# Kernel optimization log

Measured on AMD Instinct MI355X. Metric: run time of the kernel, lower is better.

Reference implementation:

```python
import jax, jax.numpy as jnp
import numpy as np

N = 50000
E = 800000
EPS = 1e-5

def _gcn_conv(x, src, dst, norm, W, b):
    # PyG GCNConv: linear transform, normalized gather/scatter, then bias.
    xw = x @ W                                   # [N, out]
    msgs = xw[src] * norm[:, None]               # [E+N, out] gather
    out = jax.ops.segment_sum(msgs, dst, num_segments=N)  # scatter-add
    return out + b

def _bn_eval(x, gamma, beta, mean, var):
    return (x - mean) * jax.lax.rsqrt(var + EPS) * gamma + beta

def setup_inputs() -> dict:
    key = jax.random.key(0)
    ks = jax.random.split(key, 24)
    dims = [(128, 256), (256, 128), (128, 64), (64, 6)]
    inp = {
        "x": jax.random.normal(ks[0], (N, 128), dtype=jnp.float32),
        "edge_index": jax.random.randint(ks[1], (2, E), 0, N, dtype=jnp.int64),
    }
    i = 2
    for li, (fi, fo) in enumerate(dims, start=1):
        scale = 1.0 / np.sqrt(fi)
        inp[f"W{li}"] = jax.random.uniform(ks[i], (fi, fo), jnp.float32, -scale, scale); i += 1
        inp[f"b{li}"] = jnp.zeros((fo,), jnp.float32)
        if li < 4:  # BN after first three convs
            inp[f"g{li}"] = jnp.ones((fo,), jnp.float32)
            inp[f"be{li}"] = jnp.zeros((fo,), jnp.float32)
            inp[f"m{li}"] = 0.1 * jax.random.normal(ks[i], (fo,), jnp.float32); i += 1
            inp[f"v{li}"] = jax.random.uniform(ks[i], (fo,), jnp.float32, 0.5, 1.5); i += 1
    return inp

def reference(x, edge_index,
              W1, b1, g1, be1, m1, v1,
              W2, b2, g2, be2, m2, v2,
              W3, b3, g3, be3, m3, v3,
              W4, b4):
    # Add self-loops once; symmetric normalization deg^-1/2 (with self-loops).
    loops = jnp.arange(N, dtype=edge_index.dtype)
    src = jnp.concatenate([edge_index[0], loops])
    dst = jnp.concatenate([edge_index[1], loops])
    deg = jax.ops.segment_sum(jnp.ones_like(dst, dtype=x.dtype), dst, num_segments=N)
    dinv = jnp.where(deg > 0, jax.lax.rsqrt(deg), 0.0)
    norm = dinv[src] * dinv[dst]  # [E+N]

    h = _gcn_conv(x, src, dst, norm, W1, b1)
    h = jax.nn.relu(_bn_eval(h, g1, be1, m1, v1))  # dropout: no-op in eval
    h = _gcn_conv(h, src, dst, norm, W2, b2)
    h = jax.nn.relu(_bn_eval(h, g2, be2, m2, v2))
    h = _gcn_conv(h, src, dst, norm, W3, b3)
    h = jax.nn.relu(_bn_eval(h, g3, be3, m3, v3))
    return _gcn_conv(h, src, dst, norm, W4, b4)
```

## Files before the change

kernel.cpp:

```cpp
#include <hip/hip_runtime.h>
#include <hip/hip_bf16.h>
#include <hip/hip_fp16.h>

#define EPS 1e-5f

constexpr int NN = 50000;
constexpr int NE = 800000;

typedef __attribute__((ext_vector_type(8))) __bf16 bf16x8;
typedef __attribute__((ext_vector_type(4))) float f32x4;

__global__ void memset_i32(int* p, int n) {
  int i = blockIdx.x * blockDim.x + threadIdx.x;
  if (i < n) p[i] = 0;
}

__global__ void deg_pos(const int* __restrict__ dst, int* __restrict__ degi,
                        unsigned char* __restrict__ pos8, int n) {
  int i = blockIdx.x * blockDim.x + threadIdx.x;
  if (i < n) pos8[i] = (unsigned char)atomicAdd(&degi[dst[i]], 1);
}

__global__ __launch_bounds__(1024) void scan1(const int* __restrict__ cnt,
                                              int* __restrict__ incl,
                                              int* __restrict__ bsum, int n) {
  __shared__ int s[1024];
  int tid = threadIdx.x;
  int i = blockIdx.x * 1024 + tid;
  int v = (i < n) ? cnt[i] : 0;
  s[tid] = v;
  __syncthreads();
  for (int off = 1; off < 1024; off <<= 1) {
    int t = (tid >= off) ? s[tid - off] : 0;
    __syncthreads();
    s[tid] += t;
    __syncthreads();
  }
  if (i < n) incl[i] = s[tid];
  if (tid == 1023) bsum[blockIdx.x] = s[1023];
}

__global__ void scan2(int* __restrict__ bsum, int nb) {
  int lane = threadIdx.x;
  int v = (lane < nb) ? bsum[lane] : 0;
  int orig = v;
  for (int off = 1; off < 64; off <<= 1) {
    int t = __shfl_up(v, off, 64);
    if (lane >= off) v += t;
  }
  if (lane < nb) bsum[lane] = v - orig;
}

__global__ __launch_bounds__(1024) void scan3(const int* __restrict__ cnt,
                                              const int* __restrict__ incl,
                                              const int* __restrict__ bsum,
                                              int* __restrict__ rp,
                                              float* __restrict__ dinv, int n) {
  int tid = threadIdx.x;
  int i = blockIdx.x * 1024 + tid;
  if (i < n) {
    rp[i + 1] = incl[i] + bsum[blockIdx.x];
    dinv[i] = rsqrtf((float)(cnt[i] + 1));
  }
  if (i == 0) rp[0] = 0;
}

__global__ void fill_kernel(const int* __restrict__ src, const int* __restrict__ dst,
                            const int* __restrict__ rp,
                            const unsigned char* __restrict__ pos8,
                            unsigned short* __restrict__ col, int n) {
  int i = blockIdx.x * blockDim.x + threadIdx.x;
  if (i < n) col[rp[dst[i]] + pos8[i]] = (unsigned short)src[i];
}

__device__ __forceinline__ void wsplit_one(const float* W, __bf16* th, __bf16* tl,
                                           int j, int K, int N) {
  int k = j / N, n = j - k * N;
  float v = W[j];
  __bf16 h = (__bf16)v;
  th[(size_t)n * K + k] = h;
  tl[(size_t)n * K + k] = (__bf16)(v - (float)h);
}

__global__ void wsplit_scale(const float* __restrict__ W1, __bf16* t1h, __bf16* t1l,
                             const float* __restrict__ W2, __bf16* t2h, __bf16* t2l,
                             const float* __restrict__ W3, __bf16* t3h, __bf16* t3l,
                             const float* __restrict__ W4, __bf16* t4h, __bf16* t4l,
                             const float* __restrict__ x, const float* __restrict__ dinv,
                             __half* __restrict__ Xh) {
  int i = blockIdx.x * blockDim.x + threadIdx.x;
  if (i < 32768) { wsplit_one(W1, t1h, t1l, i, 128, 256); return; }
  if (i < 65536) { wsplit_one(W2, t2h, t2l, i - 32768, 256, 128); return; }
  if (i < 73728) { wsplit_one(W3, t3h, t3l, i - 65536, 128, 64); return; }
  if (i < 74112) { wsplit_one(W4, t4h, t4l, i - 73728, 64, 6); return; }
  int k = i - 74112;
  if (k >= NN * 32) return;
  int v = k >> 5, f = (k & 31) * 4;
  float4 t = ((const float4*)x)[k];
  float s = dinv[v];
  __half2* d = (__half2*)(Xh + (size_t)v * 128 + f);
  d[0] = __floats2half2_rn(t.x * s, t.y * s);
  d[1] = __floats2half2_rn(t.z * s, t.w * s);
}

template <int F, int EPI>
__global__ __launch_bounds__(256, 8) void prop_half(
    const __half* __restrict__ in, const int* __restrict__ rp,
    const unsigned short* __restrict__ col,
    const float* __restrict__ dinv, const float* __restrict__ bias,
    const float* __restrict__ gam, const float* __restrict__ bet,
    const float* __restrict__ mean, const float* __restrict__ var,
    __bf16* __restrict__ out_hi, __bf16* __restrict__ out_lo, int nnodes) {
  int tid = threadIdx.x;
  int wid = tid >> 6, lane = tid & 63;
  constexpr int VEC = F / 64;
  int v = blockIdx.x * 4 + wid;
  if (v >= nnodes) return;
  int e0 = rp[v], e1 = rp[v + 1];
  float acc[VEC];
  if constexpr (VEC == 2) {
    float2 f = __half22float2(*(const __half2*)(in + (size_t)v * F + lane * 2));
    acc[0] = f.x; acc[1] = f.y;
  } else {
    acc[0] = __half2float(in[(size_t)v * F + lane]);
  }
  int e1m1 = e1 - 1;
  constexpr int D = 8;
  for (int e = e0; e < e1; e += D) {
    bool full = (e + D <= e1);
    int ss[D];
    if (full) {
#pragma unroll
      for (int u = 0; u < D; u++) ss[u] = col[e + u];
      if constexpr (VEC == 2) {
        __half2 hv[D];
#pragma unroll
        for (int u = 0; u < D; u++)
          hv[u] = *(const __half2*)(in + (size_t)ss[u] * F + lane * 2);
#pragma unroll
        for (int u = 0; u < D; u++) {
          float2 f = __half22float2(hv[u]);
          acc[0] += f.x;
          acc[1] += f.y;
        }
      } else {
        __half hv[D];
#pragma unroll
        for (int u = 0; u < D; u++) hv[u] = in[(size_t)ss[u] * F + lane];
#pragma unroll
        for (int u = 0; u < D; u++) acc[0] += __half2float(hv[u]);
      }
    } else {
      float w[D];
#pragma unroll
      for (int u = 0; u < D; u++) {
        int ei = e + u;
        ss[u] = col[ei < e1m1 ? ei : e1m1];
        w[u] = (ei < e1) ? 1.f : 0.f;
      }
      if constexpr (VEC == 2) {
        __half2 hv[D];
#pragma unroll
        for (int u = 0; u < D; u++)
          hv[u] = *(const __half2*)(in + (size_t)ss[u] * F + lane * 2);
#pragma unroll
        for (int u = 0; u < D; u++) {
          float2 f = __half22float2(hv[u]);
          acc[0] = fmaf(f.x, w[u], acc[0]);
          acc[1] = fmaf(f.y, w[u], acc[1]);
        }
      } else {
        __half hv[D];
#pragma unroll
        for (int u = 0; u < D; u++) hv[u] = in[(size_t)ss[u] * F + lane];
#pragma unroll
        for (int u = 0; u < D; u++) acc[0] = fmaf(__half2float(hv[u]), w[u], acc[0]);
      }
    }
  }
  float dv = dinv[v];
#pragma unroll
  for (int j = 0; j < VEC; j++) {
    int f = lane * VEC + j;
    float t = acc[j] * dv;
    if constexpr (EPI >= 1) {
      t += bias[f];
      t = (t - mean[f]) * rsqrtf(var[f] + EPS) * gam[f] + bet[f];
      t = fmaxf(t, 0.f);
    }
    __bf16 h = (__bf16)t;
    out_hi[(size_t)v * F + f] = h;
    out_lo[(size_t)v * F + f] = (__bf16)(t - (float)h);
  }
}

__global__ __launch_bounds__(256, 8) void prop_small(
    const float* __restrict__ in, const int* __restrict__ rp,
    const unsigned short* __restrict__ col,
    const float* __restrict__ dinv, const float* __restrict__ bias,
    float* __restrict__ out, int nnodes) {
  constexpr int F = 6;
  int tid = threadIdx.x;
  int wid = tid >> 6, lane = tid & 63;
  int g = lane >> 3, f = lane & 7;
  int v = (blockIdx.x * 4 + wid) * 8 + g;
  if (v >= nnodes || f >= F) return;
  int e0 = rp[v], e1 = rp[v + 1];
  float acc = in[(size_t)v * F + f];
  int e1m1 = e1 - 1;
  constexpr int D = 8;
  for (int e = e0; e < e1; e += D) {
    int ss[D];
    float w[D];
#pragma unroll
    for (int u = 0; u < D; u++) {
      int ei = e + u;
      ss[u] = col[ei < e1m1 ? ei : e1m1];
      w[u] = (ei < e1) ? 1.0f : 0.0f;
    }
#pragma unroll
    for (int u = 0; u < D; u++) acc = fmaf(in[(size_t)ss[u] * F + f], w[u], acc);
  }
  out[(size_t)v * F + f] = acc * dinv[v] + bias[f];
}

template <int BN, int EPI>
__global__ __launch_bounds__(256, 4) void mfma_gemm(
    const __bf16* __restrict__ Ahi, const __bf16* __restrict__ Alo,
    const __bf16* __restrict__ Bhi, const __bf16* __restrict__ Blo,
    const float* __restrict__ bias, const float* __restrict__ gam,
    const float* __restrict__ bet, const float* __restrict__ mean,
    const float* __restrict__ var, const float* __restrict__ dinv,
    float* __restrict__ Cf, __half* __restrict__ Ch,
    __bf16* __restrict__ Chi, __bf16* __restrict__ Clo,
    int M, int K, int N) {
  constexpr int BM = 128, BK = 32, NB = BN / 16;
  __shared__ __bf16 Ah[BM][BK + 8], Al[BM][BK + 8];
  __shared__ __bf16 Bh[BN][BK + 8], Bl[BN][BK + 8];
  int tid = threadIdx.x;
  int wid = tid >> 6, lane = tid & 63;
  int lr = lane & 15, lg = lane >> 4;
  int bm = blockIdx.x * BM, bn = blockIdx.y * BN;
  f32x4 acc[2][NB] = {};
  for (int k0 = 0; k0 < K; k0 += BK) {
#pragma unroll
    for (int c = 0; c < 2; c++) {
      int idx = tid + c * 256;
      int r = idx >> 2, s = idx & 3;
      int rg = bm + r;
      uint4 vh = {0, 0, 0, 0}, vl = {0, 0, 0, 0};
      if (rg < M) {
        size_t go = (size_t)rg * K + k0 + s * 8;
        vh = *reinterpret_cast<const uint4*>(Ahi + go);
        vl = *reinterpret_cast<const uint4*>(Alo + go);
      }
      *reinterpret_cast<uint4*>(&Ah[r][s * 8]) = vh;
      *reinterpret_cast<uint4*>(&Al[r][s * 8]) = vl;
    }
#pragma unroll
    for (int c = 0; c < (BN * 4 + 255) / 256; c++) {
      int idx = tid + c * 256;
      if (idx < BN * 4) {
        int r = idx >> 2, s = idx & 3;
        int rg = bn + r;
        uint4 vh = {0, 0, 0, 0}, vl = {0, 0, 0, 0};
        if (rg < N) {
          size_t go = (size_t)rg * K + k0 + s * 8;
          vh = *reinterpret_cast<const uint4*>(Bhi + go);
          vl = *reinterpret_cast<const uint4*>(Blo + go);
        }
        *reinterpret_cast<uint4*>(&Bh[r][s * 8]) = vh;
        *reinterpret_cast<uint4*>(&Bl[r][s * 8]) = vl;
      }
    }
    __syncthreads();
    int ar = wid * 32 + lr;
    bf16x8 ah0 = *reinterpret_cast<const bf16x8*>(&Ah[ar][lg * 8]);
    bf16x8 ah1 = *reinterpret_cast<const bf16x8*>(&Ah[ar + 16][lg * 8]);
    bf16x8 al0 = *reinterpret_cast<const bf16x8*>(&Al[ar][lg * 8]);
    bf16x8 al1 = *reinterpret_cast<const bf16x8*>(&Al[ar + 16][lg * 8]);
#pragma unroll
    for (int n = 0; n < NB; n++) {
      bf16x8 bh = *reinterpret_cast<const bf16x8*>(&Bh[n * 16 + lr][lg * 8]);
      bf16x8 bl = *reinterpret_cast<const bf16x8*>(&Bl[n * 16 + lr][lg * 8]);
      acc[0][n] = __builtin_amdgcn_mfma_f32_16x16x32_bf16(ah0, bh, acc[0][n], 0, 0, 0);
      acc[1][n] = __builtin_amdgcn_mfma_f32_16x16x32_bf16(ah1, bh, acc[1][n], 0, 0, 0);
      acc[0][n] = __builtin_amdgcn_mfma_f32_16x16x32_bf16(ah0, bl, acc[0][n], 0, 0, 0);
      acc[1][n] = __builtin_amdgcn_mfma_f32_16x16x32_bf16(ah1, bl, acc[1][n], 0, 0, 0);
      acc[0][n] = __builtin_amdgcn_mfma_f32_16x16x32_bf16(al0, bh, acc[0][n], 0, 0, 0);
      acc[1][n] = __builtin_amdgcn_mfma_f32_16x16x32_bf16(al1, bh, acc[1][n], 0, 0, 0);
    }
    __syncthreads();
  }
#pragma unroll
  for (int m = 0; m < 2; m++) {
    int row0 = bm + wid * 32 + m * 16 + lg * 4;
#pragma unroll
    for (int n = 0; n < NB; n++) {
      int colg = bn + n * 16 + lr;
#pragma unroll
      for (int r = 0; r < 4; r++) {
        int row = row0 + r;
        if (row >= M) continue;
        float t = acc[m][n][r];
        if constexpr (EPI == 0) {
          t += bias[colg];
          t = (t - mean[colg]) * rsqrtf(var[colg] + EPS) * gam[colg] + bet[colg];
          t = fmaxf(t, 0.f);
          __bf16 h = (__bf16)t;
          Chi[(size_t)row * N + colg] = h;
          Clo[(size_t)row * N + colg] = (__bf16)(t - (float)h);
        } else if constexpr (EPI == 1) {
          Ch[(size_t)row * N + colg] = __float2half(t * dinv[row]);
        } else {
          if (colg < N) Cf[(size_t)row * N + colg] = t * dinv[row];
        }
      }
    }
  }
}

extern "C" void kernel_launch(void* const* d_in, const int* in_sizes, int n_in,
                              void* d_out, int out_size, void* d_ws, size_t ws_size,
                              hipStream_t stream) {
  const float* x = (const float*)d_in[0];
  const int* ei = (const int*)d_in[1];
  const int* esrc = ei;
  const int* edst = ei + NE;
  const float* W1 = (const float*)d_in[2];  const float* b1 = (const float*)d_in[3];
  const float* g1 = (const float*)d_in[4];  const float* be1 = (const float*)d_in[5];
  const float* m1 = (const float*)d_in[6];  const float* v1 = (const float*)d_in[7];
  const float* W2 = (const float*)d_in[8];  const float* b2 = (const float*)d_in[9];
  const float* g2 = (const float*)d_in[10]; const float* be2 = (const float*)d_in[11];
  const float* m2 = (const float*)d_in[12]; const float* v2 = (const float*)d_in[13];
  const float* W3 = (const float*)d_in[14]; const float* b3 = (const float*)d_in[15];
  const float* g3 = (const float*)d_in[16]; const float* be3 = (const float*)d_in[17];
  const float* m3 = (const float*)d_in[18]; const float* v3 = (const float*)d_in[19];
  const float* W4 = (const float*)d_in[20]; const float* b4 = (const float*)d_in[21];
  float* out = (float*)d_out;

  char* base = (char*)d_ws;
  size_t off = 0;
  auto alloc = [&](size_t bytes) {
    void* p = base + off;
    off = (off + bytes + 255) & ~(size_t)255;
    return p;
  };
  __half* Xh = (__half*)alloc((size_t)NN * 128 * 2);
  float* F1 = (float*)alloc((size_t)NN * 6 * 4);
  __bf16* PAh = (__bf16*)alloc((size_t)NN * 128 * 2);
  __bf16* PAl = (__bf16*)alloc((size_t)NN * 128 * 2);
  __bf16* PHh = (__bf16*)alloc((size_t)NN * 256 * 2);
  __bf16* PHl = (__bf16*)alloc((size_t)NN * 256 * 2);
  __bf16* Wt1h = (__bf16*)alloc(128 * 256 * 2); __bf16* Wt1l = (__bf16*)alloc(128 * 256 * 2);
  __bf16* Wt2h = (__bf16*)alloc(256 * 128 * 2); __bf16* Wt2l = (__bf16*)alloc(256 * 128 * 2);
  __bf16* Wt3h = (__bf16*)alloc(128 * 64 * 2);  __bf16* Wt3l = (__bf16*)alloc(128 * 64 * 2);
  __bf16* Wt4h = (__bf16*)alloc(64 * 6 * 2);    __bf16* Wt4l = (__bf16*)alloc(64 * 6 * 2);
  int* degi = (int*)alloc((size_t)NN * 4);
  float* dinv = (float*)alloc((size_t)NN * 4);
  int* rp = (int*)alloc((size_t)(NN + 1) * 4);
  int* incl = (int*)alloc((size_t)NN * 4);
  int* bsum = (int*)alloc(64 * 4);
  unsigned short* col = (unsigned short*)alloc((size_t)NE * 2);
  unsigned char* pos8 = (unsigned char*)alloc((size_t)NE);

  const int nBlkN = (NN + 255) / 256;
  const int nBlkE = (NE + 255) / 256;
  const int nBlkScan = (NN + 1023) / 1024;
  const int gM = (NN + 127) / 128;
  const int gP = (NN + 3) / 4;

  memset_i32<<<nBlkN, 256, 0, stream>>>(degi, NN);
  deg_pos<<<nBlkE, 256, 0, stream>>>(edst, degi, pos8, NE);
  scan1<<<nBlkScan, 1024, 0, stream>>>(degi, incl, bsum, NN);
  scan2<<<1, 64, 0, stream>>>(bsum, nBlkScan);
  scan3<<<nBlkScan, 1024, 0, stream>>>(degi, incl, bsum, rp, dinv, NN);
  fill_kernel<<<nBlkE, 256, 0, stream>>>(esrc, edst, rp, pos8, col, NE);

  wsplit_scale<<<(74112 + NN * 32 + 255) / 256, 256, 0, stream>>>(
      W1, Wt1h, Wt1l, W2, Wt2h, Wt2l, W3, Wt3h, Wt3l, W4, Wt4h, Wt4l, x, dinv, Xh);

  prop_half<128, 0><<<gP, 256, 0, stream>>>(Xh, rp, col, dinv, nullptr, nullptr, nullptr,
                                            nullptr, nullptr, PAh, PAl, NN);
  {
    dim3 g(gM, 2);
    mfma_gemm<128, 0><<<g, 256, 0, stream>>>(PAh, PAl, Wt1h, Wt1l, b1, g1, be1, m1, v1,
                                             nullptr, nullptr, nullptr, PHh, PHl,
                                             NN, 128, 256);
  }
  {
    dim3 g(gM, 1);
    mfma_gemm<128, 1><<<g, 256, 0, stream>>>(PHh, PHl, Wt2h, Wt2l, nullptr, nullptr,
                                             nullptr, nullptr, nullptr, dinv,
                                             nullptr, Xh, nullptr, nullptr, NN, 256, 128);
  }
  prop_half<128, 1><<<gP, 256, 0, stream>>>(Xh, rp, col, dinv, b2, g2, be2, m2, v2,
                                            PAh, PAl, NN);
  {
    dim3 g(gM, 1);
    mfma_gemm<64, 1><<<g, 256, 0, stream>>>(PAh, PAl, Wt3h, Wt3l, nullptr, nullptr,
                                            nullptr, nullptr, nullptr, dinv,
                                            nullptr, Xh, nullptr, nullptr, NN, 128, 64);
  }
  prop_half<64, 1><<<gP, 256, 0, stream>>>(Xh, rp, col, dinv, b3, g3, be3, m3, v3,
                                           PHh, PHl, NN);
  {
    dim3 g(gM, 1);
    mfma_gemm<16, 2><<<g, 256, 0, stream>>>(PHh, PHl, Wt4h, Wt4l, nullptr, nullptr,
                                            nullptr, nullptr, nullptr, dinv,
                                            F1, nullptr, nullptr, nullptr, NN, 64, 6);
  }
  prop_small<<<(NN + 31) / 32, 256, 0, stream>>>(F1, rp, col, dinv, b4, out, NN);
}
```

Before: 256.6 us.

## Switch activations to single fp16 and use fp16 MFMA with split weights

After: 237.6 us. 1.08x faster.

```diff
diff --git a/kernel.cpp b/kernel.cpp
--- a/kernel.cpp
+++ b/kernel.cpp
@@ -7,7 +7,7 @@
 constexpr int NN = 50000;
 constexpr int NE = 800000;
 
-typedef __attribute__((ext_vector_type(8))) __bf16 bf16x8;
+typedef __attribute__((ext_vector_type(8))) _Float16 f16x8;
 typedef __attribute__((ext_vector_type(4))) float f32x4;
 
 __global__ void memset_i32(int* p, int n) {
@@ -73,19 +73,19 @@
   if (i < n) col[rp[dst[i]] + pos8[i]] = (unsigned short)src[i];
 }
 
-__device__ __forceinline__ void wsplit_one(const float* W, __bf16* th, __bf16* tl,
+__device__ __forceinline__ void wsplit_one(const float* W, __half* th, __half* tl,
                                            int j, int K, int N) {
   int k = j / N, n = j - k * N;
   float v = W[j];
-  __bf16 h = (__bf16)v;
+  __half h = __float2half(v);
   th[(size_t)n * K + k] = h;
-  tl[(size_t)n * K + k] = (__bf16)(v - (float)h);
-}
-
-__global__ void wsplit_scale(const float* __restrict__ W1, __bf16* t1h, __bf16* t1l,
-                             const float* __restrict__ W2, __bf16* t2h, __bf16* t2l,
-                             const float* __restrict__ W3, __bf16* t3h, __bf16* t3l,
-                             const float* __restrict__ W4, __bf16* t4h, __bf16* t4l,
+  tl[(size_t)n * K + k] = __float2half(v - __half2float(h));
+}
+
+__global__ void wsplit_scale(const float* __restrict__ W1, __half* t1h, __half* t1l,
+                             const float* __restrict__ W2, __half* t2h, __half* t2l,
+                             const float* __restrict__ W3, __half* t3h, __half* t3l,
+                             const float* __restrict__ W4, __half* t4h, __half* t4l,
                              const float* __restrict__ x, const float* __restrict__ dinv,
                              __half* __restrict__ Xh) {
   int i = blockIdx.x * blockDim.x + threadIdx.x;
@@ -110,7 +110,7 @@
     const float* __restrict__ dinv, const float* __restrict__ bias,
     const float* __restrict__ gam, const float* __restrict__ bet,
     const float* __restrict__ mean, const float* __restrict__ var,
-    __bf16* __restrict__ out_hi, __bf16* __restrict__ out_lo, int nnodes) {
+    __half* __restrict__ out_h, int nnodes) {
   int tid = threadIdx.x;
   int wid = tid >> 6, lane = tid & 63;
   constexpr int VEC = F / 64;
@@ -179,18 +179,27 @@
     }
   }
   float dv = dinv[v];
-#pragma unroll
-  for (int j = 0; j < VEC; j++) {
-    int f = lane * VEC + j;
-    float t = acc[j] * dv;
+  float t0;
+  {
+    int f = lane * VEC;
+    t0 = acc[0] * dv;
     if constexpr (EPI >= 1) {
-      t += bias[f];
-      t = (t - mean[f]) * rsqrtf(var[f] + EPS) * gam[f] + bet[f];
-      t = fmaxf(t, 0.f);
-    }
-    __bf16 h = (__bf16)t;
-    out_hi[(size_t)v * F + f] = h;
-    out_lo[(size_t)v * F + f] = (__bf16)(t - (float)h);
+      t0 += bias[f];
+      t0 = (t0 - mean[f]) * rsqrtf(var[f] + EPS) * gam[f] + bet[f];
+      t0 = fmaxf(t0, 0.f);
+    }
+  }
+  if constexpr (VEC == 2) {
+    int f = lane * 2 + 1;
+    float t1 = acc[1] * dv;
+    if constexpr (EPI >= 1) {
+      t1 += bias[f];
+      t1 = (t1 - mean[f]) * rsqrtf(var[f] + EPS) * gam[f] + bet[f];
+      t1 = fmaxf(t1, 0.f);
+    }
+    *(__half2*)(out_h + (size_t)v * F + lane * 2) = __floats2half2_rn(t0, t1);
+  } else {
+    out_h[(size_t)v * F + lane] = __float2half(t0);
   }
 }
 
@@ -226,17 +235,16 @@
 
 template <int BN, int EPI>
 __global__ __launch_bounds__(256, 4) void mfma_gemm(
-    const __bf16* __restrict__ Ahi, const __bf16* __restrict__ Alo,
-    const __bf16* __restrict__ Bhi, const __bf16* __restrict__ Blo,
+    const __half* __restrict__ A,
+    const __half* __restrict__ Bhi, const __half* __restrict__ Blo,
     const float* __restrict__ bias, const float* __restrict__ gam,
     const float* __restrict__ bet, const float* __restrict__ mean,
     const float* __restrict__ var, const float* __restrict__ dinv,
     float* __restrict__ Cf, __half* __restrict__ Ch,
-    __bf16* __restrict__ Chi, __bf16* __restrict__ Clo,
     int M, int K, int N) {
   constexpr int BM = 128, BK = 32, NB = BN / 16;
-  __shared__ __bf16 Ah[BM][BK + 8], Al[BM][BK + 8];
-  __shared__ __bf16 Bh[BN][BK + 8], Bl[BN][BK + 8];
+  __shared__ __half Ah[BM][BK + 8];
+  __shared__ __half Bh[BN][BK + 8], Bl[BN][BK + 8];
   int tid = threadIdx.x;
   int wid = tid >> 6, lane = tid & 63;
   int lr = lane & 15, lg = lane >> 4;
@@ -248,14 +256,9 @@
       int idx = tid + c * 256;
       int r = idx >> 2, s = idx & 3;
       int rg = bm + r;
-      uint4 vh = {0, 0, 0, 0}, vl = {0, 0, 0, 0};
-      if (rg < M) {
-        size_t go = (size_t)rg * K + k0 + s * 8;
-        vh = *reinterpret_cast<const uint4*>(Ahi + go);
-        vl = *reinterpret_cast<const uint4*>(Alo + go);
-      }
-      *reinterpret_cast<uint4*>(&Ah[r][s * 8]) = vh;
-      *reinterpret_cast<uint4*>(&Al[r][s * 8]) = vl;
+      uint4 va = {0, 0, 0, 0};
+      if (rg < M) va = *reinterpret_cast<const uint4*>(A + (size_t)rg * K + k0 + s * 8);
+      *reinterpret_cast<uint4*>(&Ah[r][s * 8]) = va;
     }
 #pragma unroll
     for (int c = 0; c < (BN * 4 + 255) / 256; c++) {
@@ -275,20 +278,16 @@
     }
     __syncthreads();
     int ar = wid * 32 + lr;
-    bf16x8 ah0 = *reinterpret_cast<const bf16x8*>(&Ah[ar][lg * 8]);
-    bf16x8 ah1 = *reinterpret_cast<const bf16x8*>(&Ah[ar + 16][lg * 8]);
-    bf16x8 al0 = *reinterpret_cast<const bf16x8*>(&Al[ar][lg * 8]);
-    bf16x8 al1 = *reinterpret_cast<const bf16x8*>(&Al[ar + 16][lg * 8]);
+    f16x8 a0 = *reinterpret_cast<const f16x8*>(&Ah[ar][lg * 8]);
+    f16x8 a1 = *reinterpret_cast<const f16x8*>(&Ah[ar + 16][lg * 8]);
 #pragma unroll
     for (int n = 0; n < NB; n++) {
-      bf16x8 bh = *reinterpret_cast<const bf16x8*>(&Bh[n * 16 + lr][lg * 8]);
-      bf16x8 bl = *reinterpret_cast<const bf16x8*>(&Bl[n * 16 + lr][lg * 8]);
-      acc[0][n] = __builtin_amdgcn_mfma_f32_16x16x32_bf16(ah0, bh, acc[0][n], 0, 0, 0);
-      acc[1][n] = __builtin_amdgcn_mfma_f32_16x16x32_bf16(ah1, bh, acc[1][n], 0, 0, 0);
-      acc[0][n] = __builtin_amdgcn_mfma_f32_16x16x32_bf16(ah0, bl, acc[0][n], 0, 0, 0);
-      acc[1][n] = __builtin_amdgcn_mfma_f32_16x16x32_bf16(ah1, bl, acc[1][n], 0, 0, 0);
-      acc[0][n] = __builtin_amdgcn_mfma_f32_16x16x32_bf16(al0, bh, acc[0][n], 0, 0, 0);
-      acc[1][n] = __builtin_amdgcn_mfma_f32_16x16x32_bf16(al1, bh, acc[1][n], 0, 0, 0);
+      f16x8 bh = *reinterpret_cast<const f16x8*>(&Bh[n * 16 + lr][lg * 8]);
+      f16x8 bl = *reinterpret_cast<const f16x8*>(&Bl[n * 16 + lr][lg * 8]);
+      acc[0][n] = __builtin_amdgcn_mfma_f32_16x16x32_f16(a0, bh, acc[0][n], 0, 0, 0);
+      acc[1][n] = __builtin_amdgcn_mfma_f32_16x16x32_f16(a1, bh, acc[1][n], 0, 0, 0);
+      acc[0][n] = __builtin_amdgcn_mfma_f32_16x16x32_f16(a0, bl, acc[0][n], 0, 0, 0);
+      acc[1][n] = __builtin_amdgcn_mfma_f32_16x16x32_f16(a1, bl, acc[1][n], 0, 0, 0);
     }
     __syncthreads();
   }
@@ -301,19 +300,17 @@
 #pragma unroll
       for (int r = 0; r < 4; r++) {
         int row = row0 + r;
-        if (row >= M) continue;
+        if (row >= M || colg >= N) continue;
         float t = acc[m][n][r];
         if constexpr (EPI == 0) {
           t += bias[colg];
           t = (t - mean[colg]) * rsqrtf(var[colg] + EPS) * gam[colg] + bet[colg];
           t = fmaxf(t, 0.f);
-          __bf16 h = (__bf16)t;
-          Chi[(size_t)row * N + colg] = h;
-          Clo[(size_t)row * N + colg] = (__bf16)(t - (float)h);
+          Ch[(size_t)row * N + colg] = __float2half(t);
         } else if constexpr (EPI == 1) {
           Ch[(size_t)row * N + colg] = __float2half(t * dinv[row]);
         } else {
-          if (colg < N) Cf[(size_t)row * N + colg] = t * dinv[row];
+          Cf[(size_t)row * N + colg] = t * dinv[row];
         }
       }
     }
@@ -347,15 +344,13 @@
     return p;
   };
   __half* Xh = (__half*)alloc((size_t)NN * 128 * 2);
+  __half* PA = (__half*)alloc((size_t)NN * 128 * 2);
+  __half* H  = (__half*)alloc((size_t)NN * 256 * 2);
   float* F1 = (float*)alloc((size_t)NN * 6 * 4);
-  __bf16* PAh = (__bf16*)alloc((size_t)NN * 128 * 2);
-  __bf16* PAl = (__bf16*)alloc((size_t)NN * 128 * 2);
-  __bf16* PHh = (__bf16*)alloc((size_t)NN * 256 * 2);
-  __bf16* PHl = (__bf16*)alloc((size_t)NN * 256 * 2);
-  __bf16* Wt1h = (__bf16*)alloc(128 * 256 * 2); __bf16* Wt1l = (__bf16*)alloc(128 * 256 * 2);
-  __bf16* Wt2h = (__bf16*)alloc(256 * 128 * 2); __bf16* Wt2l = (__bf16*)alloc(256 * 128 * 2);
-  __bf16* Wt3h = (__bf16*)alloc(128 * 64 * 2);  __bf16* Wt3l = (__bf16*)alloc(128 * 64 * 2);
-  __bf16* Wt4h = (__bf16*)alloc(64 * 6 * 2);    __bf16* Wt4l = (__bf16*)alloc(64 * 6 * 2);
+  __half* Wt1h = (__half*)alloc(128 * 256 * 2); __half* Wt1l = (__half*)alloc(128 * 256 * 2);
+  __half* Wt2h = (__half*)alloc(256 * 128 * 2); __half* Wt2l = (__half*)alloc(256 * 128 * 2);
+  __half* Wt3h = (__half*)alloc(128 * 64 * 2);  __half* Wt3l = (__half*)alloc(128 * 64 * 2);
+  __half* Wt4h = (__half*)alloc(64 * 6 * 2);    __half* Wt4l = (__half*)alloc(64 * 6 * 2);
   int* degi = (int*)alloc((size_t)NN * 4);
   float* dinv = (float*)alloc((size_t)NN * 4);
   int* rp = (int*)alloc((size_t)(NN + 1) * 4);
@@ -381,34 +376,33 @@
       W1, Wt1h, Wt1l, W2, Wt2h, Wt2l, W3, Wt3h, Wt3l, W4, Wt4h, Wt4l, x, dinv, Xh);
 
   prop_half<128, 0><<<gP, 256, 0, stream>>>(Xh, rp, col, dinv, nullptr, nullptr, nullptr,
-                                            nullptr, nullptr, PAh, PAl, NN);
+                                            nullptr, nullptr, PA, NN);
   {
     dim3 g(gM, 2);
-    mfma_gemm<128, 0><<<g, 256, 0, stream>>>(PAh, PAl, Wt1h, Wt1l, b1, g1, be1, m1, v1,
-                                             nullptr, nullptr, nullptr, PHh, PHl,
-                                             NN, 128, 256);
+    mfma_gemm<128, 0><<<g, 256, 0, stream>>>(PA, Wt1h, Wt1l, b1, g1, be1, m1, v1,
+                                             nullptr, nullptr, H, NN, 128, 256);
   }
   {
     dim3 g(gM, 1);
-    mfma_gemm<128, 1><<<g, 256, 0, stream>>>(PHh, PHl, Wt2h, Wt2l, nullptr, nullptr,
-                                             nullptr, nullptr, nullptr, dinv,
-                                             nullptr, Xh, nullptr, nullptr, NN, 256, 128);
+    mfma_gemm<128, 1><<<g, 256, 0, stream>>>(H, Wt2h, Wt2l, nullptr, nullptr, nullptr,
+                                             nullptr, nullptr, dinv, nullptr, Xh,
+                                             NN, 256, 128);
   }
   prop_half<128, 1><<<gP, 256, 0, stream>>>(Xh, rp, col, dinv, b2, g2, be2, m2, v2,
-                                            PAh, PAl, NN);
+                                            PA, NN);
   {
     dim3 g(gM, 1);
-    mfma_gemm<64, 1><<<g, 256, 0, stream>>>(PAh, PAl, Wt3h, Wt3l, nullptr, nullptr,
-                                            nullptr, nullptr, nullptr, dinv,
-                                            nullptr, Xh, nullptr, nullptr, NN, 128, 64);
+    mfma_gemm<64, 1><<<g, 256, 0, stream>>>(PA, Wt3h, Wt3l, nullptr, nullptr, nullptr,
+                                            nullptr, nullptr, dinv, nullptr, Xh,
+                                            NN, 128, 64);
   }
   prop_half<64, 1><<<gP, 256, 0, stream>>>(Xh, rp, col, dinv, b3, g3, be3, m3, v3,
-                                           PHh, PHl, NN);
+                                           H, NN);
   {
     dim3 g(gM, 1);
-    mfma_gemm<16, 2><<<g, 256, 0, stream>>>(PHh, PHl, Wt4h, Wt4l, nullptr, nullptr,
-                                            nullptr, nullptr, nullptr, dinv,
-                                            F1, nullptr, nullptr, nullptr, NN, 64, 6);
+    mfma_gemm<16, 2><<<g, 256, 0, stream>>>(H, Wt4h, Wt4l, nullptr, nullptr, nullptr,
+                                            nullptr, nullptr, dinv, F1, nullptr,
+                                            NN, 64, 6);
   }
   prop_small<<<(NN + 31) / 32, 256, 0, stream>>>(F1, rp, col, dinv, b4, out, NN);
 }
```
